# Kernel optimization log

Hardware: AMD Instinct MI355X
Metric: run time of the kernel (lower is better)

## Reference

```python
import jax, jax.numpy as jnp
import numpy as np

N, E, G = 100000, 3200000, 128
F, H = 9, 64


def _lin(key, fan_in, fan_out):
    s = 1.0 / np.sqrt(fan_in)
    k1, k2 = jax.random.split(key)
    W = jax.random.uniform(k1, (fan_in, fan_out), minval=-s, maxval=s, dtype=jnp.float32)
    b = jax.random.uniform(k2, (fan_out,), minval=-s, maxval=s, dtype=jnp.float32)
    return W, b


def setup_inputs() -> dict:
    key = jax.random.key(0)
    ks = jax.random.split(key, 16)
    x = jax.random.normal(ks[0], (N, F), dtype=jnp.float32)
    edge_index = jax.random.randint(ks[1], (2, E), 0, N, dtype=jnp.int64)
    edge_attr = jax.random.normal(ks[2], (E, 1), dtype=jnp.float32)
    batch = jnp.sort(jax.random.randint(ks[3], (N,), 0, G, dtype=jnp.int64))
    B_total = jax.random.uniform(ks[4], (G,), dtype=jnp.float32)
    terminal_mask = jax.random.randint(ks[5], (N,), 0, 2, dtype=jnp.int32)
    c_cost = jax.random.uniform(ks[6], (N,), dtype=jnp.float32)
    We1, be1 = _lin(ks[7], 1, F)   # GINEConv edge projection edge_dim->in_channels
    W1a, b1a = _lin(ks[8], F, H)
    W1b, b1b = _lin(ks[9], H, H)
    We2, be2 = _lin(ks[10], 1, H)
    W2a, b2a = _lin(ks[11], H, H)
    W2b, b2b = _lin(ks[12], H, H)
    Wr1, br1 = _lin(ks[13], H, H // 2)
    Wr2, br2 = _lin(ks[14], H // 2, 1)
    return dict(x=x, edge_index=edge_index, edge_attr=edge_attr, batch=batch,
                B_total=B_total, terminal_mask=terminal_mask, c_cost=c_cost,
                We1=We1, be1=be1, W1a=W1a, b1a=b1a, W1b=W1b, b1b=b1b,
                We2=We2, be2=be2, W2a=W2a, b2a=b2a, W2b=W2b, b2b=b2b,
                Wr1=Wr1, br1=br1, Wr2=Wr2, br2=br2)


def _gine_conv(h, src, dst, edge_attr, We, be, Wa, ba, Wb, bb):
    # GINEConv (eps=0): nn((1+eps)*x_i + sum_j ReLU(x_j + Lin(edge_attr)))
    ea = edge_attr @ We + be                      # [E, dim]
    msg = jax.nn.relu(h[src] + ea)                # gather + edge fuse + relu
    agg = jax.ops.segment_sum(msg, dst, num_segments=N)  # scatter-add
    z = h + agg
    z = jax.nn.relu(z @ Wa + ba)
    return jax.nn.relu(z @ Wb + bb)


def reference(x, edge_index, edge_attr, batch, B_total, terminal_mask, c_cost,
              We1, be1, W1a, b1a, W1b, b1b, We2, be2, W2a, b2a, W2b, b2b,
              Wr1, br1, Wr2, br2):
    src, dst = edge_index[0], edge_index[1]
    h = _gine_conv(x, src, dst, edge_attr, We1, be1, W1a, b1a, W1b, b1b)
    h = _gine_conv(h, src, dst, edge_attr, We2, be2, W2a, b2a, W2b, b2b)
    pi_raw = jax.nn.sigmoid(jax.nn.relu(h @ Wr1 + br1) @ Wr2 + br2)[:, 0]  # [N]
    pi_raw = pi_raw * (1.0 - terminal_mask.astype(pi_raw.dtype))
    node_expenses = pi_raw * c_cost
    total_expenses = jax.ops.segment_sum(node_expenses, batch, num_segments=B_total.shape[0])
    ratio = jnp.minimum(B_total[batch] / (total_expenses[batch] + 1e-12), 1.0)
    return pi_raw * ratio
```

## Files before the change

### kernel.cpp

```cpp
#include <hip/hip_runtime.h>
#include <hip/hip_fp16.h>
#include <math.h>

#define TPB 256
#define TPBF 1024
#define P_BLOCKS 512
#define BSHIFT 8
#define BINS_MAX 512

struct alignas(8)  h2x2 { __half2 a, b; };
struct alignas(16) h2x4 { __half2 a, b, c, d; };

typedef _Float16 f16;
typedef __attribute__((ext_vector_type(8))) _Float16 f16x8;
typedef __attribute__((ext_vector_type(4))) float f32x4;

#define MFMA16(a, b, c) __builtin_amdgcn_mfma_f32_16x16x32_f16(a, b, c, 0, 0, 0)

__global__ void __launch_bounds__(1024) k_bhist(const int* __restrict__ dst,
                                                int* __restrict__ counts, int E, int B) {
  __shared__ int h[BINS_MAX];
  int t = threadIdx.x, blk = blockIdx.x;
  for (int i = t; i < B; i += TPBF) h[i] = 0;
  __syncthreads();
  int chunk = (E + P_BLOCKS - 1) / P_BLOCKS;
  int s = blk * chunk, e = min(E, s + chunk);
  for (int i = s + t; i < e; i += TPBF)
    atomicAdd(&h[__builtin_nontemporal_load(&dst[i]) >> BSHIFT], 1);
  __syncthreads();
  for (int i = t; i < B; i += TPBF) counts[i * P_BLOCKS + blk] = h[i];
}

__global__ void k_scan_block(const int* __restrict__ deg, int* __restrict__ offs,
                             int* __restrict__ bsums, int n) {
  __shared__ int lds[256];
  int t = threadIdx.x, b = blockIdx.x;
  int base = b * 1024 + t * 4;
  int v0 = (base + 0 < n) ? deg[base + 0] : 0;
  int v1 = (base + 1 < n) ? deg[base + 1] : 0;
  int v2 = (base + 2 < n) ? deg[base + 2] : 0;
  int v3 = (base + 3 < n) ? deg[base + 3] : 0;
  int s = v0 + v1 + v2 + v3;
  lds[t] = s;
  __syncthreads();
  int acc = s;
  for (int off = 1; off < 256; off <<= 1) {
    int x = (t >= off) ? lds[t - off] : 0;
    __syncthreads();
    acc += x;
    lds[t] = acc;
    __syncthreads();
  }
  int excl = acc - s;
  if (base + 0 < n) offs[base + 0] = excl;
  if (base + 1 < n) offs[base + 1] = excl + v0;
  if (base + 2 < n) offs[base + 2] = excl + v0 + v1;
  if (base + 3 < n) offs[base + 3] = excl + v0 + v1 + v2;
  if (t == 255) bsums[b] = acc;
}

__global__ void k_scan_mid(int* __restrict__ bsums, int nb) {
  __shared__ int lds[256];
  int t = threadIdx.x;
  int v = (t < nb) ? bsums[t] : 0;
  lds[t] = v;
  __syncthreads();
  int acc = v;
  for (int off = 1; off < 256; off <<= 1) {
    int x = (t >= off) ? lds[t - off] : 0;
    __syncthreads();
    acc += x;
    lds[t] = acc;
    __syncthreads();
  }
  if (t < nb) bsums[t] = acc - v;
}

__global__ void k_scan_add(int* __restrict__ offs, const int* __restrict__ bsums,
                           int n, int total) {
  int t = threadIdx.x, b = blockIdx.x;
  int add = bsums[b];
  int base = b * 1024 + t * 4;
#pragma unroll
  for (int j = 0; j < 4; ++j)
    if (base + j < n) offs[base + j] += add;
  if (b == 0 && t == 0) offs[n] = total;
}

__global__ void __launch_bounds__(1024) k_bfill(const int* __restrict__ src,
                                                const int* __restrict__ dst,
                                                const float* __restrict__ attr,
                                                const int* __restrict__ offs,
                                                int2* __restrict__ ebuf, int E, int B) {
  __shared__ int cur[BINS_MAX];
  int t = threadIdx.x, blk = blockIdx.x;
  for (int i = t; i < B; i += TPBF) cur[i] = offs[i * P_BLOCKS + blk];
  __syncthreads();
  int chunk = (E + P_BLOCKS - 1) / P_BLOCKS;
  int s = blk * chunk, e = min(E, s + chunk);
#pragma unroll 4
  for (int i = s + t; i < e; i += TPBF) {
    int d = __builtin_nontemporal_load(&dst[i]);
    int sv = __builtin_nontemporal_load(&src[i]);
    float av = __builtin_nontemporal_load(&attr[i]);
    int bin = d >> BSHIFT;
    int pos = atomicAdd(&cur[bin], 1);
    ebuf[pos] = make_int2((sv << BSHIFT) | (d & ((1 << BSHIFT) - 1)), __float_as_int(av));
  }
}

__global__ void __launch_bounds__(1024) k_bsort(const long long* __restrict__ ebuf,
                                                const int* __restrict__ offs,
                                                int2* __restrict__ csr,
                                                int* __restrict__ noffs,
                                                int N, int E) {
  __shared__ int hist[256];
  __shared__ int cursor[256];
  __shared__ int sc[256];
  int t = threadIdx.x, bkt = blockIdx.x;
  if (t < 256) hist[t] = 0;
  __syncthreads();
  int s = offs[bkt * P_BLOCKS], e = offs[(bkt + 1) * P_BLOCKS];
#pragma unroll 4
  for (int i = s + t; i < e; i += TPBF) {
    long long pv = __builtin_nontemporal_load(&ebuf[i]);
    int key = (int)(unsigned int)(pv & 0xffffffffLL);
    atomicAdd(&hist[key & 255], 1);
  }
  __syncthreads();
  int v = (t < 256) ? hist[t] : 0;
  int acc = v;
  if (t < 256) sc[t] = v;
  __syncthreads();
  for (int off = 1; off < 256; off <<= 1) {
    int x = (t >= off && t < 256) ? sc[t - off] : 0;
    __syncthreads();
    acc += x;
    if (t < 256) sc[t] = acc;
    __syncthreads();
  }
  if (t < 256) {
    int base = s + acc - v;
    cursor[t] = base;
    int n = (bkt << BSHIFT) + t;
    if (n < N) noffs[n] = base;
  }
  if (bkt == 0 && t == 0) noffs[N] = E;
  __syncthreads();
#pragma unroll 4
  for (int i = s + t; i < e; i += TPBF) {
    long long pv = __builtin_nontemporal_load(&ebuf[i]);
    int key = (int)(unsigned int)(pv & 0xffffffffLL);
    int attr = (int)(unsigned int)(((unsigned long long)pv) >> 32);
    int pos = atomicAdd(&cursor[key & 255], 1);
    csr[pos] = make_int2(((unsigned int)key) >> BSHIFT, attr);
  }
}

__global__ void __launch_bounds__(256) k_agg1(
    const float* __restrict__ x, const int2* __restrict__ csr,
    const int* __restrict__ noffs, const float* __restrict__ We1,
    const float* __restrict__ be1, float* __restrict__ u1, int N) {
  int t = blockIdx.x * TPB + threadIdx.x;
  int node = t >> 4, f = t & 15;
  if (node >= N || f >= 9) return;
  int o0 = noffs[node], o1 = noffs[node + 1];
  float we = We1[f], be = be1[f];
  float acc = 0.f;
  int last = o1 - 1;
  for (int e = o0; e < o1; e += 8) {
    int i0 = e;     bool m0 = i0 < o1; i0 = m0 ? i0 : last;
    int i1 = e + 1; bool m1 = i1 < o1; i1 = m1 ? i1 : last;
    int i2 = e + 2; bool m2 = i2 < o1; i2 = m2 ? i2 : last;
    int i3 = e + 3; bool m3 = i3 < o1; i3 = m3 ? i3 : last;
    int i4 = e + 4; bool m4 = i4 < o1; i4 = m4 ? i4 : last;
    int i5 = e + 5; bool m5 = i5 < o1; i5 = m5 ? i5 : last;
    int i6 = e + 6; bool m6 = i6 < o1; i6 = m6 ? i6 : last;
    int i7 = e + 7; bool m7 = i7 < o1; i7 = m7 ? i7 : last;
    int2 p0 = csr[i0], p1 = csr[i1], p2 = csr[i2], p3 = csr[i3];
    int2 p4 = csr[i4], p5 = csr[i5], p6 = csr[i6], p7 = csr[i7];
    float v0 = x[p0.x * 9 + f] + fmaf(__int_as_float(p0.y), we, be);
    float v1 = x[p1.x * 9 + f] + fmaf(__int_as_float(p1.y), we, be);
    float v2 = x[p2.x * 9 + f] + fmaf(__int_as_float(p2.y), we, be);
    float v3 = x[p3.x * 9 + f] + fmaf(__int_as_float(p3.y), we, be);
    float v4 = x[p4.x * 9 + f] + fmaf(__int_as_float(p4.y), we, be);
    float v5 = x[p5.x * 9 + f] + fmaf(__int_as_float(p5.y), we, be);
    float v6 = x[p6.x * 9 + f] + fmaf(__int_as_float(p6.y), we, be);
    float v7 = x[p7.x * 9 + f] + fmaf(__int_as_float(p7.y), we, be);
    acc += m0 ? fmaxf(v0, 0.f) : 0.f;
    acc += m1 ? fmaxf(v1, 0.f) : 0.f;
    acc += m2 ? fmaxf(v2, 0.f) : 0.f;
    acc += m3 ? fmaxf(v3, 0.f) : 0.f;
    acc += m4 ? fmaxf(v4, 0.f) : 0.f;
    acc += m5 ? fmaxf(v5, 0.f) : 0.f;
    acc += m6 ? fmaxf(v6, 0.f) : 0.f;
    acc += m7 ? fmaxf(v7, 0.f) : 0.f;
  }
  u1[node * 9 + f] = x[node * 9 + f] + acc;
}

__global__ void __launch_bounds__(256) k_agg2(
    const __half* __restrict__ h1, const long long* __restrict__ csr,
    const int* __restrict__ noffs, const float* __restrict__ We2,
    const float* __restrict__ be2, float* __restrict__ u2, int n_base, int n_end) {
  int gt = blockIdx.x * TPB + threadIdx.x;
  int node = n_base + (gt >> 6);
  if (node >= n_end) return;
  int lane = gt & 63;
  int q = lane >> 3, c = lane & 7;
  float4 weA = *(const float4*)&We2[c * 8];
  float4 weB = *(const float4*)&We2[c * 8 + 4];
  float4 beA = *(const float4*)&be2[c * 8];
  float4 beB = *(const float4*)&be2[c * 8 + 4];
  int o0 = noffs[node], o1 = noffs[node + 1];
  float a0 = 0.f, a1 = 0.f, a2 = 0.f, a3 = 0.f, a4 = 0.f, a5 = 0.f, a6 = 0.f, a7 = 0.f;

#define AGG2_ACCM(pv, v, m)                                                  \
  {                                                                          \
    float ea = __int_as_float((int)(unsigned int)(((unsigned long long)(pv)) >> 32)); \
    float2 f0 = __half22float2((v).a), f1 = __half22float2((v).b);           \
    float2 f2 = __half22float2((v).c), f3 = __half22float2((v).d);           \
    a0 += (m) ? fmaxf(f0.x + fmaf(ea, weA.x, beA.x), 0.f) : 0.f;             \
    a1 += (m) ? fmaxf(f0.y + fmaf(ea, weA.y, beA.y), 0.f) : 0.f;             \
    a2 += (m) ? fmaxf(f1.x + fmaf(ea, weA.z, beA.z), 0.f) : 0.f;             \
    a3 += (m) ? fmaxf(f1.y + fmaf(ea, weA.w, beA.w), 0.f) : 0.f;             \
    a4 += (m) ? fmaxf(f2.x + fmaf(ea, weB.x, beB.x), 0.f) : 0.f;             \
    a5 += (m) ? fmaxf(f2.y + fmaf(ea, weB.y, beB.y), 0.f) : 0.f;             \
    a6 += (m) ? fmaxf(f3.x + fmaf(ea, weB.z, beB.z), 0.f) : 0.f;             \
    a7 += (m) ? fmaxf(f3.y + fmaf(ea, weB.w, beB.w), 0.f) : 0.f;             \
  }

  int e = o0;
  if (o1 - e > 32) {
    int last = o1 - 1;
    do {
      long long pv0, pv1, pv2, pv3, pv4, pv5, pv6, pv7;
      bool m0, m1, m2, m3, m4, m5, m6, m7;
      {
        int i0 = e + q;      m0 = i0 < o1; i0 = m0 ? i0 : last;
        int i1 = e + 8 + q;  m1 = i1 < o1; i1 = m1 ? i1 : last;
        int i2 = e + 16 + q; m2 = i2 < o1; i2 = m2 ? i2 : last;
        int i3 = e + 24 + q; m3 = i3 < o1; i3 = m3 ? i3 : last;
        int i4 = e + 32 + q; m4 = i4 < o1; i4 = m4 ? i4 : last;
        int i5 = e + 40 + q; m5 = i5 < o1; i5 = m5 ? i5 : last;
        int i6 = e + 48 + q; m6 = i6 < o1; i6 = m6 ? i6 : last;
        int i7 = e + 56 + q; m7 = i7 < o1; i7 = m7 ? i7 : last;
        pv0 = __builtin_nontemporal_load(&csr[i0]);
        pv1 = __builtin_nontemporal_load(&csr[i1]);
        pv2 = __builtin_nontemporal_load(&csr[i2]);
        pv3 = __builtin_nontemporal_load(&csr[i3]);
        pv4 = __builtin_nontemporal_load(&csr[i4]);
        pv5 = __builtin_nontemporal_load(&csr[i5]);
        pv6 = __builtin_nontemporal_load(&csr[i6]);
        pv7 = __builtin_nontemporal_load(&csr[i7]);
      }
      h2x4 v0 = *(const h2x4*)(h1 + (size_t)(int)(unsigned int)(pv0 & 0xffffffffLL) * 64 + c * 8);
      h2x4 v1 = *(const h2x4*)(h1 + (size_t)(int)(unsigned int)(pv1 & 0xffffffffLL) * 64 + c * 8);
      h2x4 v2 = *(const h2x4*)(h1 + (size_t)(int)(unsigned int)(pv2 & 0xffffffffLL) * 64 + c * 8);
      h2x4 v3 = *(const h2x4*)(h1 + (size_t)(int)(unsigned int)(pv3 & 0xffffffffLL) * 64 + c * 8);
      h2x4 v4 = *(const h2x4*)(h1 + (size_t)(int)(unsigned int)(pv4 & 0xffffffffLL) * 64 + c * 8);
      h2x4 v5 = *(const h2x4*)(h1 + (size_t)(int)(unsigned int)(pv5 & 0xffffffffLL) * 64 + c * 8);
      h2x4 v6 = *(const h2x4*)(h1 + (size_t)(int)(unsigned int)(pv6 & 0xffffffffLL) * 64 + c * 8);
      h2x4 v7 = *(const h2x4*)(h1 + (size_t)(int)(unsigned int)(pv7 & 0xffffffffLL) * 64 + c * 8);
      AGG2_ACCM(pv0, v0, m0); AGG2_ACCM(pv1, v1, m1);
      AGG2_ACCM(pv2, v2, m2); AGG2_ACCM(pv3, v3, m3);
      AGG2_ACCM(pv4, v4, m4); AGG2_ACCM(pv5, v5, m5);
      AGG2_ACCM(pv6, v6, m6); AGG2_ACCM(pv7, v7, m7);
      e += 64;
    } while (o1 - e > 32);
  }
  if (e < o1) {
    int last = o1 - 1;
    int i0 = e + q;      bool m0 = i0 < o1; i0 = m0 ? i0 : last;
    int i1 = e + 8 + q;  bool m1 = i1 < o1; i1 = m1 ? i1 : last;
    int i2 = e + 16 + q; bool m2 = i2 < o1; i2 = m2 ? i2 : last;
    int i3 = e + 24 + q; bool m3 = i3 < o1; i3 = m3 ? i3 : last;
    long long pv0 = __builtin_nontemporal_load(&csr[i0]);
    long long pv1 = __builtin_nontemporal_load(&csr[i1]);
    long long pv2 = __builtin_nontemporal_load(&csr[i2]);
    long long pv3 = __builtin_nontemporal_load(&csr[i3]);
    h2x4 v0 = *(const h2x4*)(h1 + (size_t)(int)(unsigned int)(pv0 & 0xffffffffLL) * 64 + c * 8);
    h2x4 v1 = *(const h2x4*)(h1 + (size_t)(int)(unsigned int)(pv1 & 0xffffffffLL) * 64 + c * 8);
    h2x4 v2 = *(const h2x4*)(h1 + (size_t)(int)(unsigned int)(pv2 & 0xffffffffLL) * 64 + c * 8);
    h2x4 v3 = *(const h2x4*)(h1 + (size_t)(int)(unsigned int)(pv3 & 0xffffffffLL) * 64 + c * 8);
    AGG2_ACCM(pv0, v0, m0); AGG2_ACCM(pv1, v1, m1);
    AGG2_ACCM(pv2, v2, m2); AGG2_ACCM(pv3, v3, m3);
  }
#undef AGG2_ACCM

  a0 += __shfl_xor(a0, 8, 64); a0 += __shfl_xor(a0, 16, 64); a0 += __shfl_xor(a0, 32, 64);
  a1 += __shfl_xor(a1, 8, 64); a1 += __shfl_xor(a1, 16, 64); a1 += __shfl_xor(a1, 32, 64);
  a2 += __shfl_xor(a2, 8, 64); a2 += __shfl_xor(a2, 16, 64); a2 += __shfl_xor(a2, 32, 64);
  a3 += __shfl_xor(a3, 8, 64); a3 += __shfl_xor(a3, 16, 64); a3 += __shfl_xor(a3, 32, 64);
  a4 += __shfl_xor(a4, 8, 64); a4 += __shfl_xor(a4, 16, 64); a4 += __shfl_xor(a4, 32, 64);
  a5 += __shfl_xor(a5, 8, 64); a5 += __shfl_xor(a5, 16, 64); a5 += __shfl_xor(a5, 32, 64);
  a6 += __shfl_xor(a6, 8, 64); a6 += __shfl_xor(a6, 16, 64); a6 += __shfl_xor(a6, 32, 64);
  a7 += __shfl_xor(a7, 8, 64); a7 += __shfl_xor(a7, 16, 64); a7 += __shfl_xor(a7, 32, 64);

  if (q == 0) {
    h2x4 sf = *(const h2x4*)(h1 + (size_t)node * 64 + c * 8);
    float2 s0 = __half22float2(sf.a), s1 = __half22float2(sf.b);
    float2 s2 = __half22float2(sf.c), s3 = __half22float2(sf.d);
    float4 oA, oB;
    oA.x = s0.x + a0; oA.y = s0.y + a1; oA.z = s1.x + a2; oA.w = s1.y + a3;
    oB.x = s2.x + a4; oB.y = s2.y + a5; oB.z = s3.x + a6; oB.w = s3.y + a7;
    *(float4*)&u2[(size_t)node * 64 + c * 8] = oA;
    *(float4*)&u2[(size_t)node * 64 + c * 8 + 4] = oB;
  }
}

__device__ __forceinline__ void splitf8(const float* v, f16x8& h, f16x8& l) {
#pragma unroll
  for (int j = 0; j < 8; ++j) {
    float x = v[j];
    f16 hh = (f16)x;
    h[j] = hh;
    l[j] = (f16)(x - (float)hh);
  }
}

__device__ __forceinline__ void pack_w(const float* __restrict__ W, int Ntiles, int nslots,
                                       f16* hi, f16* lo, int t) {
  int lane = t & 63;
  int kg = lane >> 4, m = lane & 15;
  int Nout = Ntiles * 16;
  for (int s = t >> 6; s < nslots; s += 4) {
    int ks = s / Ntiles, nt = s - ks * Ntiles;
    int kbase = ks * 32 + kg * 8;
    int n = nt * 16 + m;
    float v[8];
#pragma unroll
    for (int j = 0; j < 8; ++j) v[j] = W[(kbase + j) * Nout + n];
    f16x8 h, l;
    splitf8(v, h, l);
    *(f16x8*)&hi[(s * 64 + lane) * 8] = h;
    *(f16x8*)&lo[(s * 64 + lane) * 8] = l;
  }
}

__global__ void __launch_bounds__(256) k_mlp9(
    const float* __restrict__ uin, const float* __restrict__ Wa,
    const float* __restrict__ ba, const float* __restrict__ Wb,
    const float* __restrict__ bb, __half* __restrict__ hout, int N) {
  __shared__ __align__(16) f16 wf1h[2048], wf1l[2048];
  __shared__ __align__(16) f16 wf2h[4096], wf2l[4096];
  __shared__ float ls_z[64 * 65];
  __shared__ float ls_ba[64], ls_bb[64];
  const int t = threadIdx.x;
  const int n0 = blockIdx.x * 64;
  const int w = t >> 6, lane = t & 63;
  const int m = lane & 15, kg = lane >> 4;

  {
    int s = w;
    int n = s * 16 + m;
    float v[8];
#pragma unroll
    for (int j = 0; j < 8; ++j) {
      int k = kg * 8 + j;
      v[j] = (k < 9) ? Wa[k * 64 + n] : 0.f;
    }
    f16x8 h, l;
    splitf8(v, h, l);
    *(f16x8*)&wf1h[(s * 64 + lane) * 8] = h;
    *(f16x8*)&wf1l[(s * 64 + lane) * 8] = l;
  }
  pack_w(Wb, 4, 8, wf2h, wf2l, t);
  if (t < 64) { ls_ba[t] = ba[t]; ls_bb[t] = bb[t]; }
  __syncthreads();

  int row = min(n0 + w * 16 + m, N - 1);
  float av[8];
#pragma unroll
  for (int j = 0; j < 8; ++j) {
    int k = kg * 8 + j;
    av[j] = (k < 9) ? uin[(size_t)row * 9 + k] : 0.f;
  }
  f16x8 a0h, a0l, a1h, a1l;
  splitf8(av, a0h, a0l);

  f32x4 acc[4];
#pragma unroll
  for (int nt = 0; nt < 4; ++nt) { f32x4 z4 = {0.f, 0.f, 0.f, 0.f}; acc[nt] = z4; }
#pragma unroll
  for (int nt = 0; nt < 4; ++nt) {
    f16x8 bh = *(const f16x8*)&wf1h[(nt * 64 + lane) * 8];
    f16x8 bl = *(const f16x8*)&wf1l[(nt * 64 + lane) * 8];
    acc[nt] = MFMA16(a0h, bh, acc[nt]);
    acc[nt] = MFMA16(a0l, bh, acc[nt]);
    acc[nt] = MFMA16(a0h, bl, acc[nt]);
  }
#pragma unroll
  for (int nt = 0; nt < 4; ++nt)
#pragma unroll
    for (int r = 0; r < 4; ++r)
      ls_z[(w * 16 + kg * 4 + r) * 65 + nt * 16 + m] = fmaxf(acc[nt][r] + ls_ba[nt * 16 + m], 0.f);
  __syncthreads();

  const float* zr = &ls_z[(size_t)(w * 16 + m) * 65 + kg * 8];
  {
    float zv0[8], zv1[8];
#pragma unroll
    for (int j = 0; j < 8; ++j) { zv0[j] = zr[j]; zv1[j] = zr[32 + j]; }
    splitf8(zv0, a0h, a0l);
    splitf8(zv1, a1h, a1l);
  }
#pragma unroll
  for (int nt = 0; nt < 4; ++nt) { f32x4 z4 = {0.f, 0.f, 0.f, 0.f}; acc[nt] = z4; }
#pragma unroll
  for (int nt = 0; nt < 4; ++nt) {
#pragma unroll
    for (int ks = 0; ks < 2; ++ks) {
      int s = ks * 4 + nt;
      f16x8 bh = *(const f16x8*)&wf2h[(s * 64 + lane) * 8];
      f16x8 bl = *(const f16x8*)&wf2l[(s * 64 + lane) * 8];
      f16x8 ah = ks ? a1h : a0h;
      f16x8 al = ks ? a1l : a0l;
      acc[nt] = MFMA16(ah, bh, acc[nt]);
      acc[nt] = MFMA16(al, bh, acc[nt]);
      acc[nt] = MFMA16(ah, bl, acc[nt]);
    }
  }
#pragma unroll
  for (int nt = 0; nt < 4; ++nt)
#pragma unroll
    for (int r = 0; r < 4; ++r) {
      int node = n0 + w * 16 + kg * 4 + r;
      if (node < N)
        hout[(size_t)node * 64 + nt * 16 + m] =
            __float2half(fmaxf(acc[nt][r] + ls_bb[nt * 16 + m], 0.f));
    }
}

__global__ void __launch_bounds__(256) k_mlp_ro(
    const float* __restrict__ uin, const float* __restrict__ Wa,
    const float* __restrict__ ba, const float* __restrict__ Wb,
    const float* __restrict__ bb, const float* __restrict__ Wr1,
    const float* __restrict__ br1, const float* __restrict__ Wr2,
    const float* __restrict__ br2, const int* __restrict__ tmask,
    float* __restrict__ pi, int N) {
  __shared__ __align__(16) f16 wf1h[4096], wf1l[4096];
  __shared__ __align__(16) f16 wf2h[4096], wf2l[4096];
  __shared__ __align__(16) f16 wfrh[2048], wfrl[2048];
  __shared__ float ls_z[64 * 65];
  __shared__ float ls_ba[64], ls_bb[64], ls_br1[32], ls_w2[32];
  const int t = threadIdx.x;
  const int n0 = blockIdx.x * 64;

  pack_w(Wa, 4, 8, wf1h, wf1l, t);
  pack_w(Wb, 4, 8, wf2h, wf2l, t);
  pack_w(Wr1, 2, 4, wfrh, wfrl, t);
  if (t < 64) { ls_ba[t] = ba[t]; ls_bb[t] = bb[t]; }
  else if (t < 96) { ls_br1[t - 64] = br1[t - 64]; ls_w2[t - 64] = Wr2[t - 64]; }
  __syncthreads();

  const int w = t >> 6, lane = t & 63;
  const int m = lane & 15, kg = lane >> 4;

  int row = n0 + w * 16 + m;
  row = min(row, N - 1);
  const float* ar = uin + (size_t)row * 64 + kg * 8;
  float av0[8], av1[8];
  {
    f32x4 p0 = *(const f32x4*)ar;
    f32x4 p1 = *(const f32x4*)(ar + 4);
    f32x4 p2 = *(const f32x4*)(ar + 32);
    f32x4 p3 = *(const f32x4*)(ar + 36);
#pragma unroll
    for (int j = 0; j < 4; ++j) {
      av0[j] = p0[j]; av0[4 + j] = p1[j];
      av1[j] = p2[j]; av1[4 + j] = p3[j];
    }
  }
  f16x8 a0h, a0l, a1h, a1l;
  splitf8(av0, a0h, a0l);
  splitf8(av1, a1h, a1l);

  f32x4 acc[4];
#pragma unroll
  for (int nt = 0; nt < 4; ++nt) { f32x4 z4 = {0.f, 0.f, 0.f, 0.f}; acc[nt] = z4; }
#pragma unroll
  for (int nt = 0; nt < 4; ++nt) {
#pragma unroll
    for (int ks = 0; ks < 2; ++ks) {
      int s = ks * 4 + nt;
      f16x8 bh = *(const f16x8*)&wf1h[(s * 64 + lane) * 8];
      f16x8 bl = *(const f16x8*)&wf1l[(s * 64 + lane) * 8];
      f16x8 ah = ks ? a1h : a0h;
      f16x8 al = ks ? a1l : a0l;
      acc[nt] = MFMA16(ah, bh, acc[nt]);
      acc[nt] = MFMA16(al, bh, acc[nt]);
      acc[nt] = MFMA16(ah, bl, acc[nt]);
    }
  }
#pragma unroll
  for (int nt = 0; nt < 4; ++nt)
#pragma unroll
    for (int r = 0; r < 4; ++r)
      ls_z[(w * 16 + kg * 4 + r) * 65 + nt * 16 + m] = fmaxf(acc[nt][r] + ls_ba[nt * 16 + m], 0.f);
  __syncthreads();

  const float* zr = &ls_z[(size_t)(w * 16 + m) * 65 + kg * 8];
  {
    float zv0[8], zv1[8];
#pragma unroll
    for (int j = 0; j < 8; ++j) { zv0[j] = zr[j]; zv1[j] = zr[32 + j]; }
    splitf8(zv0, a0h, a0l);
    splitf8(zv1, a1h, a1l);
  }
#pragma unroll
  for (int nt = 0; nt < 4; ++nt) { f32x4 z4 = {0.f, 0.f, 0.f, 0.f}; acc[nt] = z4; }
#pragma unroll
  for (int nt = 0; nt < 4; ++nt) {
#pragma unroll
    for (int ks = 0; ks < 2; ++ks) {
      int s = ks * 4 + nt;
      f16x8 bh = *(const f16x8*)&wf2h[(s * 64 + lane) * 8];
      f16x8 bl = *(const f16x8*)&wf2l[(s * 64 + lane) * 8];
      f16x8 ah = ks ? a1h : a0h;
      f16x8 al = ks ? a1l : a0l;
      acc[nt] = MFMA16(ah, bh, acc[nt]);
      acc[nt] = MFMA16(al, bh, acc[nt]);
      acc[nt] = MFMA16(ah, bl, acc[nt]);
    }
  }
  __syncthreads();
#pragma unroll
  for (int nt = 0; nt < 4; ++nt)
#pragma unroll
    for (int r = 0; r < 4; ++r)
      ls_z[(w * 16 + kg * 4 + r) * 65 + nt * 16 + m] = fmaxf(acc[nt][r] + ls_bb[nt * 16 + m], 0.f);
  __syncthreads();

  {
    float zv0[8], zv1[8];
#pragma unroll
    for (int j = 0; j < 8; ++j) { zv0[j] = zr[j]; zv1[j] = zr[32 + j]; }
    splitf8(zv0, a0h, a0l);
    splitf8(zv1, a1h, a1l);
  }
  f32x4 accr[2];
#pragma unroll
  for (int nt = 0; nt < 2; ++nt) { f32x4 z4 = {0.f, 0.f, 0.f, 0.f}; accr[nt] = z4; }
#pragma unroll
  for (int nt = 0; nt < 2; ++nt) {
#pragma unroll
    for (int ks = 0; ks < 2; ++ks) {
      int s = ks * 2 + nt;
      f16x8 bh = *(const f16x8*)&wfrh[(s * 64 + lane) * 8];
      f16x8 bl = *(const f16x8*)&wfrl[(s * 64 + lane) * 8];
      f16x8 ah = ks ? a1h : a0h;
      f16x8 al = ks ? a1l : a0l;
      accr[nt] = MFMA16(ah, bh, accr[nt]);
      accr[nt] = MFMA16(al, bh, accr[nt]);
      accr[nt] = MFMA16(ah, bl, accr[nt]);
    }
  }
  float b2 = br2[0];
#pragma unroll
  for (int r = 0; r < 4; ++r) {
    float v0 = fmaxf(accr[0][r] + ls_br1[m], 0.f) * ls_w2[m];
    float v1 = fmaxf(accr[1][r] + ls_br1[16 + m], 0.f) * ls_w2[16 + m];
    float tr = v0 + v1;
    tr += __shfl_xor(tr, 1, 64);
    tr += __shfl_xor(tr, 2, 64);
    tr += __shfl_xor(tr, 4, 64);
    tr += __shfl_xor(tr, 8, 64);
    if (m == 0) {
      int node = n0 + w * 16 + kg * 4 + r;
      if (node < N) {
        float sg = 1.f / (1.f + expf(-(tr + b2)));
        pi[node] = sg * (1.f - (float)tmask[node]);
      }
    }
  }
}

__global__ void k_grpsum(const float* __restrict__ pi, const float* __restrict__ c_cost,
                         const int* __restrict__ batch, float* __restrict__ exp_tot, int N) {
  __shared__ float lsf[256];
  __shared__ int lsi[256];
  int t = threadIdx.x;
  int i = blockIdx.x * TPB + t;
  bool valid = i < N;
  int g = valid ? batch[i] : 0;
  float v = valid ? pi[i] * c_cost[i] : 0.f;
  lsi[t] = valid ? g : 0x7fffffff;
  __syncthreads();
  for (int s = 128; s > 0; s >>= 1) { if (t < s) lsi[t] = min(lsi[t], lsi[t + s]); __syncthreads(); }
  int gmin = lsi[0];
  __syncthreads();
  lsi[t] = valid ? g : -1;
  __syncthreads();
  for (int s = 128; s > 0; s >>= 1) { if (t < s) lsi[t] = max(lsi[t], lsi[t + s]); __syncthreads(); }
  int gmax = lsi[0];
  __syncthreads();
  for (int gg = gmin; gg <= gmax; ++gg) {
    lsf[t] = (valid && g == gg) ? v : 0.f;
    __syncthreads();
    for (int s = 128; s > 0; s >>= 1) { if (t < s) lsf[t] += lsf[t + s]; __syncthreads(); }
    if (t == 0) atomicAdd(&exp_tot[gg], lsf[0]);
    __syncthreads();
  }
}

__global__ void k_final(const float* __restrict__ pi, const int* __restrict__ batch,
                        const float* __restrict__ B_total, const float* __restrict__ exp_tot,
                        float* __restrict__ out, int N) {
  int i = blockIdx.x * TPB + threadIdx.x;
  if (i < N) {
    int g = batch[i];
    float ratio = fminf(B_total[g] / (exp_tot[g] + 1e-12f), 1.f);
    out[i] = pi[i] * ratio;
  }
}

extern "C" void kernel_launch(void* const* d_in, const int* in_sizes, int n_in,
                              void* d_out, int out_size, void* d_ws, size_t ws_size,
                              hipStream_t stream) {
  const float* x     = (const float*)d_in[0];
  const int*   ei    = (const int*)d_in[1];
  const float* eattr = (const float*)d_in[2];
  const int*   batch = (const int*)d_in[3];
  const float* Btot  = (const float*)d_in[4];
  const int*   tmask = (const int*)d_in[5];
  const float* ccost = (const float*)d_in[6];
  const float* We1 = (const float*)d_in[7],  *be1 = (const float*)d_in[8];
  const float* W1a = (const float*)d_in[9],  *b1a = (const float*)d_in[10];
  const float* W1b = (const float*)d_in[11], *b1b = (const float*)d_in[12];
  const float* We2 = (const float*)d_in[13], *be2 = (const float*)d_in[14];
  const float* W2a = (const float*)d_in[15], *b2a = (const float*)d_in[16];
  const float* W2b = (const float*)d_in[17], *b2b = (const float*)d_in[18];
  const float* Wr1 = (const float*)d_in[19], *br1 = (const float*)d_in[20];
  const float* Wr2 = (const float*)d_in[21], *br2 = (const float*)d_in[22];
  float* out = (float*)d_out;

  const int N = in_sizes[0] / 9;
  const int E = in_sizes[2];
  const int G = in_sizes[4];
  const int* src = ei;
  const int* dst = ei + E;
  const int B = (N + (1 << BSHIFT) - 1) >> BSHIFT;
  const int nscan = B * P_BLOCKS;

  size_t cur = 0;
  auto alloc = [&](size_t elems) { size_t r = cur; cur += elems; cur = (cur + 63) & ~(size_t)63; return r; };
  char* wsb = (char*)d_ws;
  size_t o_exp    = alloc(G);
  size_t o_counts = alloc(nscan);
  size_t o_offs   = alloc(nscan + 1);
  size_t o_bsums  = alloc(256);
  size_t o_noffs  = alloc(N + 1);
  size_t o_csr    = alloc(2 * (size_t)E);
  size_t e_or_h   = (2 * (size_t)E > (size_t)N * 32) ? 2 * (size_t)E : (size_t)N * 32;
  size_t o_ebuf   = alloc(e_or_h);
  size_t o_u1     = alloc((size_t)N * 9);
  size_t o_u2     = alloc((size_t)N * 64);
  size_t o_pi     = alloc(N);
  (void)ws_size;

  float* exp_t  = (float*)wsb + o_exp;
  int*   counts = (int*)wsb + o_counts;
  int*   offs   = (int*)wsb + o_offs;
  int*   bsums  = (int*)wsb + o_bsums;
  int*   noffs  = (int*)wsb + o_noffs;
  int2*  csr    = (int2*)((int*)wsb + o_csr);
  int2*  ebuf   = (int2*)((int*)wsb + o_ebuf);
  __half* h1h   = (__half*)((int*)wsb + o_ebuf);
  float* u1     = (float*)wsb + o_u1;
  float* u2     = (float*)wsb + o_u2;
  float* pi     = (float*)wsb + o_pi;

  (void)hipMemsetAsync(exp_t, 0, (size_t)G * 4, stream);

  const int nb = (nscan + 1023) / 1024;

  k_bhist<<<P_BLOCKS, TPBF, 0, stream>>>(dst, counts, E, B);
  k_scan_block<<<nb, TPB, 0, stream>>>(counts, offs, bsums, nscan);
  k_scan_mid<<<1, 256, 0, stream>>>(bsums, nb);
  k_scan_add<<<nb, TPB, 0, stream>>>(offs, bsums, nscan, E);
  k_bfill<<<P_BLOCKS, TPBF, 0, stream>>>(src, dst, eattr, offs, ebuf, E, B);
  k_bsort<<<B, TPBF, 0, stream>>>((const long long*)ebuf, offs, csr, noffs, N, E);

  k_agg1<<<((size_t)N * 16 + TPB - 1) / TPB, TPB, 0, stream>>>(x, csr, noffs, We1, be1, u1, N);
  k_mlp9<<<(N + 63) / 64, TPB, 0, stream>>>(u1, W1a, b1a, W1b, b1b, h1h, N);

  k_agg2<<<((size_t)N * 64 + TPB - 1) / TPB, TPB, 0, stream>>>(
      h1h, (const long long*)csr, noffs, We2, be2, u2, 0, N);

  k_mlp_ro<<<(N + 63) / 64, TPB, 0, stream>>>(u2, W2a, b2a, W2b, b2b, Wr1, br1, Wr2, br2, tmask, pi, N);

  k_grpsum<<<(N + TPB - 1) / TPB, TPB, 0, stream>>>(pi, ccost, batch, exp_t, N);
  k_final<<<(N + TPB - 1) / TPB, TPB, 0, stream>>>(pi, batch, Btot, exp_t, out, N);
}
```

Baseline: 384.5 us.

## Compute per-node degrees in histogram pass and drop bucket-sort counting pass

```diff
diff --git a/kernel.cpp b/kernel.cpp
--- a/kernel.cpp
+++ b/kernel.cpp
@@ -18,15 +18,19 @@
 #define MFMA16(a, b, c) __builtin_amdgcn_mfma_f32_16x16x32_f16(a, b, c, 0, 0, 0)
 
 __global__ void __launch_bounds__(1024) k_bhist(const int* __restrict__ dst,
-                                                int* __restrict__ counts, int E, int B) {
+                                                int* __restrict__ counts,
+                                                int* __restrict__ pdeg, int E, int B) {
   __shared__ int h[BINS_MAX];
   int t = threadIdx.x, blk = blockIdx.x;
   for (int i = t; i < B; i += TPBF) h[i] = 0;
   __syncthreads();
   int chunk = (E + P_BLOCKS - 1) / P_BLOCKS;
   int s = blk * chunk, e = min(E, s + chunk);
-  for (int i = s + t; i < e; i += TPBF)
-    atomicAdd(&h[__builtin_nontemporal_load(&dst[i]) >> BSHIFT], 1);
+  for (int i = s + t; i < e; i += TPBF) {
+    int d = __builtin_nontemporal_load(&dst[i]);
+    atomicAdd(&h[d >> BSHIFT], 1);
+    atomicAdd(&pdeg[d], 1);
+  }
   __syncthreads();
   for (int i = t; i < B; i += TPBF) counts[i * P_BLOCKS + blk] = h[i];
 }
@@ -109,44 +113,18 @@
   }
 }
 
-__global__ void __launch_bounds__(1024) k_bsort(const long long* __restrict__ ebuf,
-                                                const int* __restrict__ offs,
-                                                int2* __restrict__ csr,
-                                                int* __restrict__ noffs,
-                                                int N, int E) {
-  __shared__ int hist[256];
+__global__ void __launch_bounds__(1024) k_bsort_b(const long long* __restrict__ ebuf,
+                                                  const int* __restrict__ offs,
+                                                  const int* __restrict__ noffs,
+                                                  int2* __restrict__ csr, int N) {
   __shared__ int cursor[256];
-  __shared__ int sc[256];
   int t = threadIdx.x, bkt = blockIdx.x;
-  if (t < 256) hist[t] = 0;
+  if (t < 256) {
+    int n = (bkt << BSHIFT) + t;
+    cursor[t] = (n < N) ? noffs[n] : 0;
+  }
   __syncthreads();
   int s = offs[bkt * P_BLOCKS], e = offs[(bkt + 1) * P_BLOCKS];
-#pragma unroll 4
-  for (int i = s + t; i < e; i += TPBF) {
-    long long pv = __builtin_nontemporal_load(&ebuf[i]);
-    int key = (int)(unsigned int)(pv & 0xffffffffLL);
-    atomicAdd(&hist[key & 255], 1);
-  }
-  __syncthreads();
-  int v = (t < 256) ? hist[t] : 0;
-  int acc = v;
-  if (t < 256) sc[t] = v;
-  __syncthreads();
-  for (int off = 1; off < 256; off <<= 1) {
-    int x = (t >= off && t < 256) ? sc[t - off] : 0;
-    __syncthreads();
-    acc += x;
-    if (t < 256) sc[t] = acc;
-    __syncthreads();
-  }
-  if (t < 256) {
-    int base = s + acc - v;
-    cursor[t] = base;
-    int n = (bkt << BSHIFT) + t;
-    if (n < N) noffs[n] = base;
-  }
-  if (bkt == 0 && t == 0) noffs[N] = E;
-  __syncthreads();
 #pragma unroll 4
   for (int i = s + t; i < e; i += TPBF) {
     long long pv = __builtin_nontemporal_load(&ebuf[i]);
@@ -650,6 +628,7 @@
   size_t o_counts = alloc(nscan);
   size_t o_offs   = alloc(nscan + 1);
   size_t o_bsums  = alloc(256);
+  size_t o_pdeg   = alloc(N);
   size_t o_noffs  = alloc(N + 1);
   size_t o_csr    = alloc(2 * (size_t)E);
   size_t e_or_h   = (2 * (size_t)E > (size_t)N * 32) ? 2 * (size_t)E : (size_t)N * 32;
@@ -663,6 +642,7 @@
   int*   counts = (int*)wsb + o_counts;
   int*   offs   = (int*)wsb + o_offs;
   int*   bsums  = (int*)wsb + o_bsums;
+  int*   pdeg   = (int*)wsb + o_pdeg;
   int*   noffs  = (int*)wsb + o_noffs;
   int2*  csr    = (int2*)((int*)wsb + o_csr);
   int2*  ebuf   = (int2*)((int*)wsb + o_ebuf);
@@ -672,15 +652,21 @@
   float* pi     = (float*)wsb + o_pi;
 
   (void)hipMemsetAsync(exp_t, 0, (size_t)G * 4, stream);
-
-  const int nb = (nscan + 1023) / 1024;
-
-  k_bhist<<<P_BLOCKS, TPBF, 0, stream>>>(dst, counts, E, B);
-  k_scan_block<<<nb, TPB, 0, stream>>>(counts, offs, bsums, nscan);
-  k_scan_mid<<<1, 256, 0, stream>>>(bsums, nb);
-  k_scan_add<<<nb, TPB, 0, stream>>>(offs, bsums, nscan, E);
+  (void)hipMemsetAsync(pdeg, 0, (size_t)N * 4, stream);
+
+  const int nb1 = (nscan + 1023) / 1024;
+  const int nb2 = (N + 1023) / 1024;
+
+  k_bhist<<<P_BLOCKS, TPBF, 0, stream>>>(dst, counts, pdeg, E, B);
+  k_scan_block<<<nb1, TPB, 0, stream>>>(counts, offs, bsums, nscan);
+  k_scan_mid<<<1, 256, 0, stream>>>(bsums, nb1);
+  k_scan_add<<<nb1, TPB, 0, stream>>>(offs, bsums, nscan, E);
+  k_scan_block<<<nb2, TPB, 0, stream>>>(pdeg, noffs, bsums, N);
+  k_scan_mid<<<1, 256, 0, stream>>>(bsums, nb2);
+  k_scan_add<<<nb2, TPB, 0, stream>>>(noffs, bsums, N, E);
+
   k_bfill<<<P_BLOCKS, TPBF, 0, stream>>>(src, dst, eattr, offs, ebuf, E, B);
-  k_bsort<<<B, TPBF, 0, stream>>>((const long long*)ebuf, offs, csr, noffs, N, E);
+  k_bsort_b<<<B, TPBF, 0, stream>>>((const long long*)ebuf, offs, noffs, csr, N);
 
   k_agg1<<<((size_t)N * 16 + TPB - 1) / TPB, TPB, 0, stream>>>(x, csr, noffs, We1, be1, u1, N);
   k_mlp9<<<(N + 63) / 64, TPB, 0, stream>>>(u1, W1a, b1a, W1b, b1b, h1h, N);
```

Result: slower. 505.3 us (+31.4%).
